# Kernel optimization log

Hardware: AMD Instinct MI355X
Metric: run time of the kernel (lower is better)

The kernel has to match this reference:

```python
import jax, jax.numpy as jnp
import numpy as np

B, LX, LY, D = 8, 128, 512, 256


def setup_inputs() -> dict:
    key = jax.random.key(0)
    k = jax.random.split(key, 7)
    s1 = 1.0 / np.sqrt(2 * D)
    s2 = 1.0 / np.sqrt(D)
    return {
        "x": jax.random.normal(k[0], (B, LX, D), dtype=jnp.float32),
        "y": jax.random.normal(k[1], (B, LY, D), dtype=jnp.float32),
        "y_mask": jax.random.randint(k[2], (B, LY), 0, 2).astype(bool),
        "W1": jax.random.uniform(k[3], (2 * D, D), jnp.float32, -s1, s1),
        "b1": jax.random.uniform(k[4], (D,), jnp.float32, -s1, s1),
        "W2": jax.random.uniform(k[5], (D, 1), jnp.float32, -s2, s2),
        "b2": jax.random.uniform(k[6], (1,), jnp.float32, -s2, s2),
    }


def reference(x, y, y_mask, W1, b1, W2, b2):
    # Algebraically split the first linear on the concat [x; y]:
    # cat([x,y]) @ W1 == x @ W1[:D] + y @ W1[D:]
    d = x.shape[-1]
    hx = jnp.einsum('bxd,de->bxe', x, W1[:d])            # (B, LX, D)
    hy = jnp.einsum('byd,de->bye', y, W1[d:])            # (B, LY, D)
    h = jax.nn.relu(hx[:, :, None, :] + hy[:, None, :, :] + b1)  # (B, LX, LY, D)
    scores = jnp.einsum('bxyd,d->bxy', h, W2[:, 0]) + b2[0]      # (B, LX, LY)
    scores = jnp.where(y_mask[:, None, :], -jnp.inf, scores)
    weights = jax.nn.softmax(scores, axis=2)
    contexts = jnp.einsum('bxy,byd->bxd', weights, y)    # (B, LX, D)
    return contexts
```

## Files before the change

kernel.cpp:

```cpp
#include <hip/hip_runtime.h>
#include <math.h>

#define BB 8
#define LX 128
#define LY 512
#define DD 256

#define A_ELEMS    (BB * LX * DD)
#define CT2_OFF    A_ELEMS
#define CT2_ELEMS  (BB * (DD / 4) * LY * 4)
#define PART_OFF   (CT2_OFF + CT2_ELEMS)
#define PART_ELEMS (BB * 16 * 8 * 8 * DD)
#define PML_OFF    (PART_OFF + PART_ELEMS)

__global__ __launch_bounds__(256) void gemm_kernel(
    const float* __restrict__ x, const float* __restrict__ y,
    const float* __restrict__ W1, const float* __restrict__ b1,
    float* __restrict__ ws)
{
    __shared__ float sA[32][20];
    __shared__ float sW[32][128];

    const int g  = blockIdx.x;
    const int t  = threadIdx.x;
    const int tc = t & 31;
    const int tr = t >> 5;

    const bool isA = (g < 128);
    const float* inp;
    const float* wbase;
    int row0, col0;
    if (isA) { col0 = (g & 1) * 128;  row0 = (g >> 1) * 16;  inp = x; wbase = W1; }
    else     { int h = g - 128; col0 = (h & 1) * 128; row0 = (h >> 1) * 16; inp = y; wbase = W1 + DD * DD; }

    float acc[2][4];
    #pragma unroll
    for (int i = 0; i < 2; ++i)
        #pragma unroll
        for (int j = 0; j < 4; ++j) acc[i][j] = 0.f;

    for (int k0 = 0; k0 < DD; k0 += 32) {
        __syncthreads();
        if (t < 128) {
            int row = t >> 3, kq = t & 7;
            const float4 v = *(const float4*)(inp + (size_t)(row0 + row) * DD + k0 + 4 * kq);
            sA[4*kq + 0][row] = v.x;
            sA[4*kq + 1][row] = v.y;
            sA[4*kq + 2][row] = v.z;
            sA[4*kq + 3][row] = v.w;
        }
        #pragma unroll
        for (int i = 0; i < 4; ++i) {
            int flat = t + i * 256;
            int kk = flat >> 5, c4 = flat & 31;
            *(float4*)&sW[kk][4*c4] = *(const float4*)(wbase + (size_t)(k0 + kk) * DD + col0 + 4 * c4);
        }
        __syncthreads();
        #pragma unroll
        for (int k = 0; k < 32; ++k) {
            const float a0 = sA[k][2*tr], a1 = sA[k][2*tr + 1];
            const float4 w4 = *(const float4*)&sW[k][4*tc];
            acc[0][0] = fmaf(a0, w4.x, acc[0][0]);
            acc[0][1] = fmaf(a0, w4.y, acc[0][1]);
            acc[0][2] = fmaf(a0, w4.z, acc[0][2]);
            acc[0][3] = fmaf(a0, w4.w, acc[0][3]);
            acc[1][0] = fmaf(a1, w4.x, acc[1][0]);
            acc[1][1] = fmaf(a1, w4.y, acc[1][1]);
            acc[1][2] = fmaf(a1, w4.z, acc[1][2]);
            acc[1][3] = fmaf(a1, w4.w, acc[1][3]);
        }
    }

    if (isA) {
        const float4 bv = *(const float4*)(b1 + col0 + 4 * tc);
        #pragma unroll
        for (int i = 0; i < 2; ++i) {
            const int r = row0 + 2 * tr + i;
            float4 o;
            o.x = acc[i][0] + bv.x; o.y = acc[i][1] + bv.y;
            o.z = acc[i][2] + bv.z; o.w = acc[i][3] + bv.w;
            *(float4*)(ws + (size_t)r * DD + col0 + 4 * tc) = o;
        }
    } else {
        const int dq = (col0 >> 2) + tc;
        #pragma unroll
        for (int i = 0; i < 2; ++i) {
            const int ry = row0 + 2 * tr + i;
            const int bb = ry >> 9, yy = ry & 511;
            float4 o = {acc[i][0], acc[i][1], acc[i][2], acc[i][3]};
            *(float4*)(ws + CT2_OFF + (((size_t)(bb * 64 + dq) * 512 + yy) << 2)) = o;
        }
    }
}

__global__ __launch_bounds__(256) void score_kernel(
    const float* __restrict__ yin, const int* __restrict__ ymask,
    const float* __restrict__ W2, const float* __restrict__ b2,
    const float* __restrict__ Ain, const float* __restrict__ Ct,
    float* __restrict__ part, float* __restrict__ pml)
{
    const int t    = threadIdx.x;
    const int lane = t & 63;
    const int w    = __builtin_amdgcn_readfirstlane(t >> 6);
    const int b    = blockIdx.x & 7;
    const int r    = blockIdx.x >> 3;
    const int xg   = r & 15;
    const int yc   = r >> 4;
    const int y    = yc * 64 + lane;
    const int row0 = xg * 8 + w * 2;

    const bool msk = ymask[(size_t)b * LY + y] != 0;

    const float4* A4  = (const float4*)(Ain + ((size_t)b * LX + row0) * DD);
    const float4* W24 = (const float4*)W2;
    const float4* ct  = (const float4*)Ct + ((size_t)b * 64) * 512 + y;
    const float b2v = b2[0];

    float s0a = 0.f, s0b = 0.f, s1a = 0.f, s1b = 0.f;

    #pragma unroll 4
    for (int dq = 0; dq < 64; ++dq) {
        const float4 c  = ct[(size_t)dq * 512];
        const float4 w4 = W24[dq];
        const float4 a0 = A4[dq];
        const float4 a1 = A4[dq + 64];
        s0a = fmaf(fmaxf(a0.x + c.x, 0.f), w4.x, s0a);
        s0b = fmaf(fmaxf(a0.y + c.y, 0.f), w4.y, s0b);
        s0a = fmaf(fmaxf(a0.z + c.z, 0.f), w4.z, s0a);
        s0b = fmaf(fmaxf(a0.w + c.w, 0.f), w4.w, s0b);
        s1a = fmaf(fmaxf(a1.x + c.x, 0.f), w4.x, s1a);
        s1b = fmaf(fmaxf(a1.y + c.y, 0.f), w4.y, s1b);
        s1a = fmaf(fmaxf(a1.z + c.z, 0.f), w4.z, s1a);
        s1b = fmaf(fmaxf(a1.w + c.w, 0.f), w4.w, s1b);
    }

    const float p0 = msk ? 0.f : __expf(s0a + s0b + b2v);
    const float p1 = msk ? 0.f : __expf(s1a + s1b + b2v);

    float l0 = p0, l1 = p1;
    #pragma unroll
    for (int off = 32; off; off >>= 1) {
        l0 += __shfl_xor(l0, off);
        l1 += __shfl_xor(l1, off);
    }

    const int pi0 = __float_as_int(p0);
    const int pi1 = __float_as_int(p1);
    float4 acc0 = {0.f, 0.f, 0.f, 0.f}, acc1 = {0.f, 0.f, 0.f, 0.f};
    const float4* yb4 = (const float4*)(yin + ((size_t)b * LY + yc * 64) * DD) + lane;

    #pragma unroll 8
    for (int yy = 0; yy < 64; ++yy) {
        const float4 v = yb4[(size_t)yy * 64];
        const float q0 = __int_as_float(__builtin_amdgcn_readlane(pi0, yy));
        const float q1 = __int_as_float(__builtin_amdgcn_readlane(pi1, yy));
        acc0.x = fmaf(q0, v.x, acc0.x); acc0.y = fmaf(q0, v.y, acc0.y);
        acc0.z = fmaf(q0, v.z, acc0.z); acc0.w = fmaf(q0, v.w, acc0.w);
        acc1.x = fmaf(q1, v.x, acc1.x); acc1.y = fmaf(q1, v.y, acc1.y);
        acc1.z = fmaf(q1, v.z, acc1.z); acc1.w = fmaf(q1, v.w, acc1.w);
    }

    float* pb = part + (((size_t)(b * 16 + xg) * 8 + yc) * 8 + 2 * w) * DD;
    *(float4*)(pb + 4 * lane)      = acc0;
    *(float4*)(pb + DD + 4 * lane) = acc1;
    if (lane == 0) {
        float* ml = pml + ((size_t)(b * 16 + xg) * 8 + yc) * 8 + 2 * w;
        ml[0] = l0;
        ml[1] = l1;
    }
}

__global__ __launch_bounds__(256) void combine_kernel(
    const float* __restrict__ part, const float* __restrict__ pml,
    float* __restrict__ out)
{
    const int t = threadIdx.x;
    const int b = blockIdx.x & 7;
    const int x = blockIdx.x >> 3;
    const int xg = x >> 3, xi = x & 7;

    const size_t base = (size_t)(b * 16 + xg) * 64 + xi;

    float L = 0.f;
    #pragma unroll
    for (int c = 0; c < 8; ++c) L += pml[base + 8 * c];

    float acc = 0.f;
    #pragma unroll
    for (int c = 0; c < 8; ++c)
        acc += part[(base + 8 * c) * DD + t];

    out[((size_t)(b * LX + x)) * DD + t] = acc / L;
}

extern "C" void kernel_launch(void* const* d_in, const int* in_sizes, int n_in,
                              void* d_out, int out_size, void* d_ws, size_t ws_size,
                              hipStream_t stream) {
    const float* x     = (const float*)d_in[0];
    const float* y     = (const float*)d_in[1];
    const int*   ymask = (const int*)  d_in[2];
    const float* W1    = (const float*)d_in[3];
    const float* b1    = (const float*)d_in[4];
    const float* W2    = (const float*)d_in[5];
    const float* b2    = (const float*)d_in[6];
    float* ws  = (float*)d_ws;
    float* out = (float*)d_out;

    hipLaunchKernelGGL(gemm_kernel, dim3(640), dim3(256), 0, stream, x, y, W1, b1, ws);
    hipLaunchKernelGGL(score_kernel, dim3(1024), dim3(256), 0, stream,
                       y, ymask, W2, b2, ws, ws + CT2_OFF, ws + PART_OFF, ws + PML_OFF);
    hipLaunchKernelGGL(combine_kernel, dim3(1024), dim3(256), 0, stream,
                       ws + PART_OFF, ws + PML_OFF, out);
}
```

Before: 47.78 us.

## Use packed fp16 scores with dot2 and retile score kernel to 8 rows

The GEMM epilogue now stores the projected x and y activations and W2 as packed fp16 in an interleaved layout. The score kernel computes relu(a+c) with packed half adds and max, and accumulates with fdot2. Each wave now handles 8 x-rows over 32 y values instead of 2 rows over 64, which increases reuse of each loaded Ct and y vector, halves the grid and halves the partial slices. The aim is to cut VALU work and memory traffic in the score phase. The cost is fp16 rounding error in the scores and higher register pressure from 8 float4 accumulators.

```diff
diff --git a/kernel.cpp b/kernel.cpp
--- a/kernel.cpp
+++ b/kernel.cpp
@@ -6,17 +6,32 @@
 #define LY 512
 #define DD 256
 
-#define A_ELEMS    (BB * LX * DD)
-#define CT2_OFF    A_ELEMS
-#define CT2_ELEMS  (BB * (DD / 4) * LY * 4)
-#define PART_OFF   (CT2_OFF + CT2_ELEMS)
-#define PART_ELEMS (BB * 16 * 8 * 8 * DD)
-#define PML_OFF    (PART_OFF + PART_ELEMS)
+typedef _Float16 h2t __attribute__((ext_vector_type(2)));
+
+static __device__ __forceinline__ h2t u2h(unsigned int u) {
+    h2t r; __builtin_memcpy(&r, &u, 4); return r;
+}
+static __device__ __forceinline__ unsigned int pk16(float a, float b) {
+    h2t h; h.x = (_Float16)a; h.y = (_Float16)b;
+    unsigned int u; __builtin_memcpy(&u, &h, 4); return u;
+}
+
+#if defined(__has_builtin) && __has_builtin(__builtin_amdgcn_fdot2)
+#define DOT2(a, b, c) __builtin_amdgcn_fdot2((a), (b), (c), false)
+#else
+#define DOT2(a, b, c) fmaf((float)(a).x, (float)(b).x, fmaf((float)(a).y, (float)(b).y, (c)))
+#endif
+
+#define A16_OFF  0
+#define CT16_OFF 131072
+#define W16_OFF  655360
+#define PART_OFF 655488
+#define PML_OFF  4849792
 
 __global__ __launch_bounds__(256) void gemm_kernel(
     const float* __restrict__ x, const float* __restrict__ y,
     const float* __restrict__ W1, const float* __restrict__ b1,
-    float* __restrict__ ws)
+    const float* __restrict__ W2, float* __restrict__ ws)
 {
     __shared__ float sA[32][20];
     __shared__ float sW[32][128];
@@ -71,102 +86,127 @@
         }
     }
 
+    const int dq = (col0 >> 2) + tc;
     if (isA) {
+        uint2* A16u2 = (uint2*)(ws + A16_OFF);
         const float4 bv = *(const float4*)(b1 + col0 + 4 * tc);
         #pragma unroll
         for (int i = 0; i < 2; ++i) {
             const int r = row0 + 2 * tr + i;
-            float4 o;
-            o.x = acc[i][0] + bv.x; o.y = acc[i][1] + bv.y;
-            o.z = acc[i][2] + bv.z; o.w = acc[i][3] + bv.w;
-            *(float4*)(ws + (size_t)r * DD + col0 + 4 * tc) = o;
+            uint2 st;
+            st.x = pk16(acc[i][0] + bv.x, acc[i][1] + bv.y);
+            st.y = pk16(acc[i][2] + bv.z, acc[i][3] + bv.w);
+            A16u2[((size_t)r * 32 + (dq & 31)) * 2 + (dq >> 5)] = st;
+        }
+        if (g == 0 && t < 64) {
+            uint2* W16u2 = (uint2*)(ws + W16_OFF);
+            const float4 wv = *(const float4*)(W2 + 4 * t);
+            uint2 st;
+            st.x = pk16(wv.x, wv.y);
+            st.y = pk16(wv.z, wv.w);
+            W16u2[((t & 31)) * 2 + (t >> 5)] = st;
         }
     } else {
-        const int dq = (col0 >> 2) + tc;
+        uint2* Ct16u2 = (uint2*)(ws + CT16_OFF);
         #pragma unroll
         for (int i = 0; i < 2; ++i) {
             const int ry = row0 + 2 * tr + i;
             const int bb = ry >> 9, yy = ry & 511;
-            float4 o = {acc[i][0], acc[i][1], acc[i][2], acc[i][3]};
-            *(float4*)(ws + CT2_OFF + (((size_t)(bb * 64 + dq) * 512 + yy) << 2)) = o;
+            uint2 st;
+            st.x = pk16(acc[i][0], acc[i][1]);
+            st.y = pk16(acc[i][2], acc[i][3]);
+            Ct16u2[((size_t)(bb * 64 + dq)) * 512 + yy] = st;
         }
     }
 }
 
 __global__ __launch_bounds__(256) void score_kernel(
     const float* __restrict__ yin, const int* __restrict__ ymask,
-    const float* __restrict__ W2, const float* __restrict__ b2,
-    const float* __restrict__ Ain, const float* __restrict__ Ct,
+    const float* __restrict__ b2,
+    const uint4* __restrict__ A16, const uint2* __restrict__ Ct,
+    const uint4* __restrict__ W16,
     float* __restrict__ part, float* __restrict__ pml)
 {
     const int t    = threadIdx.x;
     const int lane = t & 63;
     const int w    = __builtin_amdgcn_readfirstlane(t >> 6);
     const int b    = blockIdx.x & 7;
-    const int r    = blockIdx.x >> 3;
-    const int xg   = r & 15;
-    const int yc   = r >> 4;
-    const int y    = yc * 64 + lane;
-    const int row0 = xg * 8 + w * 2;
+    const int r2   = blockIdx.x >> 3;
+    const int xg   = r2 & 15;
+    const int yc   = r2 >> 4;
+    const int ylo  = lane & 31;
+    const bool hi  = (lane >> 5) != 0;
+    const int y    = yc * 128 + w * 32 + ylo;
+    const int grow0 = b * LX + xg * 8;
+
+    const uint2* ctp = Ct + ((size_t)(b * 64 + (hi ? 32 : 0))) * 512 + y;
+    const uint4* A8  = A16 + (size_t)grow0 * 32;
+    const float  b2v = b2[0];
+
+    h2t zz; zz.x = (_Float16)0.f; zz.y = (_Float16)0.f;
+    float sA[8], sB[8];
+    #pragma unroll
+    for (int r = 0; r < 8; ++r) { sA[r] = 0.f; sB[r] = 0.f; }
+
+    #pragma unroll 2
+    for (int dqi = 0; dqi < 32; ++dqi) {
+        const uint2 cu = ctp[(size_t)dqi * 512];
+        const h2t c0 = u2h(cu.x), c1 = u2h(cu.y);
+        const uint4 wv = W16[dqi];
+        const h2t w0 = u2h(hi ? wv.z : wv.x);
+        const h2t w1 = u2h(hi ? wv.w : wv.y);
+        #pragma unroll
+        for (int r = 0; r < 8; ++r) {
+            const uint4 av = A8[r * 32 + dqi];
+            const h2t a0 = u2h(hi ? av.z : av.x);
+            const h2t a1 = u2h(hi ? av.w : av.y);
+            const h2t h0 = __builtin_elementwise_max(a0 + c0, zz);
+            const h2t h1 = __builtin_elementwise_max(a1 + c1, zz);
+            sA[r] = DOT2(h0, w0, sA[r]);
+            sB[r] = DOT2(h1, w1, sB[r]);
+        }
+    }
 
     const bool msk = ymask[(size_t)b * LY + y] != 0;
-
-    const float4* A4  = (const float4*)(Ain + ((size_t)b * LX + row0) * DD);
-    const float4* W24 = (const float4*)W2;
-    const float4* ct  = (const float4*)Ct + ((size_t)b * 64) * 512 + y;
-    const float b2v = b2[0];
-
-    float s0a = 0.f, s0b = 0.f, s1a = 0.f, s1b = 0.f;
-
+    float p[8]; int pi[8]; float l[8];
+    #pragma unroll
+    for (int r = 0; r < 8; ++r) {
+        float s = sA[r] + sB[r];
+        s += __shfl_xor(s, 32);
+        p[r] = msk ? 0.f : __expf(s + b2v);
+        pi[r] = __float_as_int(p[r]);
+        float lv = p[r];
+        #pragma unroll
+        for (int off = 16; off; off >>= 1) lv += __shfl_xor(lv, off);
+        l[r] = lv;
+    }
+
+    float4 acc[8];
+    #pragma unroll
+    for (int r = 0; r < 8; ++r) acc[r] = make_float4(0.f, 0.f, 0.f, 0.f);
+
+    const float4* yb = (const float4*)yin + ((size_t)(b * LY + yc * 128 + w * 32)) * 64 + lane;
     #pragma unroll 4
-    for (int dq = 0; dq < 64; ++dq) {
-        const float4 c  = ct[(size_t)dq * 512];
-        const float4 w4 = W24[dq];
-        const float4 a0 = A4[dq];
-        const float4 a1 = A4[dq + 64];
-        s0a = fmaf(fmaxf(a0.x + c.x, 0.f), w4.x, s0a);
-        s0b = fmaf(fmaxf(a0.y + c.y, 0.f), w4.y, s0b);
-        s0a = fmaf(fmaxf(a0.z + c.z, 0.f), w4.z, s0a);
-        s0b = fmaf(fmaxf(a0.w + c.w, 0.f), w4.w, s0b);
-        s1a = fmaf(fmaxf(a1.x + c.x, 0.f), w4.x, s1a);
-        s1b = fmaf(fmaxf(a1.y + c.y, 0.f), w4.y, s1b);
-        s1a = fmaf(fmaxf(a1.z + c.z, 0.f), w4.z, s1a);
-        s1b = fmaf(fmaxf(a1.w + c.w, 0.f), w4.w, s1b);
-    }
-
-    const float p0 = msk ? 0.f : __expf(s0a + s0b + b2v);
-    const float p1 = msk ? 0.f : __expf(s1a + s1b + b2v);
-
-    float l0 = p0, l1 = p1;
-    #pragma unroll
-    for (int off = 32; off; off >>= 1) {
-        l0 += __shfl_xor(l0, off);
-        l1 += __shfl_xor(l1, off);
-    }
-
-    const int pi0 = __float_as_int(p0);
-    const int pi1 = __float_as_int(p1);
-    float4 acc0 = {0.f, 0.f, 0.f, 0.f}, acc1 = {0.f, 0.f, 0.f, 0.f};
-    const float4* yb4 = (const float4*)(yin + ((size_t)b * LY + yc * 64) * DD) + lane;
-
-    #pragma unroll 8
-    for (int yy = 0; yy < 64; ++yy) {
-        const float4 v = yb4[(size_t)yy * 64];
-        const float q0 = __int_as_float(__builtin_amdgcn_readlane(pi0, yy));
-        const float q1 = __int_as_float(__builtin_amdgcn_readlane(pi1, yy));
-        acc0.x = fmaf(q0, v.x, acc0.x); acc0.y = fmaf(q0, v.y, acc0.y);
-        acc0.z = fmaf(q0, v.z, acc0.z); acc0.w = fmaf(q0, v.w, acc0.w);
-        acc1.x = fmaf(q1, v.x, acc1.x); acc1.y = fmaf(q1, v.y, acc1.y);
-        acc1.z = fmaf(q1, v.z, acc1.z); acc1.w = fmaf(q1, v.w, acc1.w);
-    }
-
-    float* pb = part + (((size_t)(b * 16 + xg) * 8 + yc) * 8 + 2 * w) * DD;
-    *(float4*)(pb + 4 * lane)      = acc0;
-    *(float4*)(pb + DD + 4 * lane) = acc1;
+    for (int yy = 0; yy < 32; ++yy) {
+        const float4 v = yb[(size_t)yy * 64];
+        #pragma unroll
+        for (int r = 0; r < 8; ++r) {
+            const float q = __int_as_float(__builtin_amdgcn_readlane(pi[r], yy));
+            acc[r].x = fmaf(q, v.x, acc[r].x);
+            acc[r].y = fmaf(q, v.y, acc[r].y);
+            acc[r].z = fmaf(q, v.z, acc[r].z);
+            acc[r].w = fmaf(q, v.w, acc[r].w);
+        }
+    }
+
+    const size_t pw = (((size_t)(b * 16 + xg) * 4 + yc) * 4 + w);
+    float* pb = part + pw * 8 * DD;
+    #pragma unroll
+    for (int r = 0; r < 8; ++r)
+        *(float4*)(pb + (size_t)r * DD + 4 * lane) = acc[r];
     if (lane == 0) {
-        float* ml = pml + ((size_t)(b * 16 + xg) * 8 + yc) * 8 + 2 * w;
-        ml[0] = l0;
-        ml[1] = l1;
+        #pragma unroll
+        for (int r = 0; r < 8; ++r) pml[pw * 8 + r] = l[r];
     }
 }
 
@@ -179,17 +219,14 @@
     const int x = blockIdx.x >> 3;
     const int xg = x >> 3, xi = x & 7;
 
-    const size_t base = (size_t)(b * 16 + xg) * 64 + xi;
-
     float L = 0.f;
-    #pragma unroll
-    for (int c = 0; c < 8; ++c) L += pml[base + 8 * c];
-
     float acc = 0.f;
     #pragma unroll
-    for (int c = 0; c < 8; ++c)
-        acc += part[(base + 8 * c) * DD + t];
-
+    for (int c = 0; c < 16; ++c) {
+        const size_t idx = (((size_t)(b * 16 + xg) * 4 + (c >> 2)) * 4 + (c & 3)) * 8 + xi;
+        L   += pml[idx];
+        acc += part[idx * DD + t];
+    }
     out[((size_t)(b * LX + x)) * DD + t] = acc / L;
 }
 
@@ -206,9 +243,12 @@
     float* ws  = (float*)d_ws;
     float* out = (float*)d_out;
 
-    hipLaunchKernelGGL(gemm_kernel, dim3(640), dim3(256), 0, stream, x, y, W1, b1, ws);
-    hipLaunchKernelGGL(score_kernel, dim3(1024), dim3(256), 0, stream,
-                       y, ymask, W2, b2, ws, ws + CT2_OFF, ws + PART_OFF, ws + PML_OFF);
+    hipLaunchKernelGGL(gemm_kernel, dim3(640), dim3(256), 0, stream, x, y, W1, b1, W2, ws);
+    hipLaunchKernelGGL(score_kernel, dim3(512), dim3(256), 0, stream,
+                       y, ymask, b2,
+                       (const uint4*)(ws + A16_OFF), (const uint2*)(ws + CT16_OFF),
+                       (const uint4*)(ws + W16_OFF),
+                       ws + PART_OFF, ws + PML_OFF);
     hipLaunchKernelGGL(combine_kernel, dim3(1024), dim3(256), 0, stream,
                        ws + PART_OFF, ws + PML_OFF, out);
 }
```

After: 50.41 us. 5.5% more time.
